# Performance work log

Measured on AMD Instinct MI355X. Metric: run time of the kernel, lower is better.

Reference implementation:

```python
import jax, jax.numpy as jnp
import numpy as np

B, S, DIM, NH, NKV, HD, HID, L, VOCAB = 1, 2048, 1024, 16, 8, 64, 2816, 2, 32000
EPS = 1e-5
SCALE = float(HD) ** 0.5
NEG = -255.0  # mask fill value used by executorch example inputs


def setup_inputs() -> dict:
    key = jax.random.key(0)
    ks = jax.random.split(key, 16)
    sd = 0.02
    def rnd(k, shape):
        return jax.random.normal(k, shape, dtype=jnp.float32) * sd
    # rope tables: precompute_freqs_cis(head_dim, max_seq_len)[: -1] -> [S, HD//2]
    inv = 1.0 / (10000.0 ** (np.arange(0, HD, 2, dtype=np.float32) / HD))
    ang = np.outer(np.arange(S, dtype=np.float32), inv)
    # causal mask [S, S]
    tril = np.tril(np.ones((S, S), dtype=bool))
    mask = np.where(tril, 0.0, NEG).astype(np.float32)
    return {
        "tokens": jax.random.randint(ks[0], (B, S), 0, VOCAB, dtype=jnp.int32),
        "atten_mask": jnp.asarray(mask),
        "freqs_cos": jnp.asarray(np.cos(ang)),
        "freqs_sin": jnp.asarray(np.sin(ang)),
        "tok_emb": rnd(ks[1], (VOCAB, DIM)),
        "wq": rnd(ks[2], (L, DIM, NH * HD)),
        "wk": rnd(ks[3], (L, DIM, NKV * HD)),
        "wv": rnd(ks[4], (L, DIM, NKV * HD)),
        "wo": rnd(ks[5], (L, NH * HD, DIM)),
        "attn_norm_w": jnp.ones((L, DIM), jnp.float32),
        "ffn_norm_w": jnp.ones((L, DIM), jnp.float32),
        "w1": rnd(ks[6], (L, DIM, HID)),
        "w2": rnd(ks[7], (L, HID, DIM)),
        "w3": rnd(ks[8], (L, DIM, HID)),
        "final_norm_w": jnp.ones((DIM,), jnp.float32),
        "out_w": rnd(ks[9], (DIM, VOCAB)),
    }


def _rmsnorm(x, w):
    return x * jax.lax.rsqrt(jnp.mean(x * x, axis=-1, keepdims=True) + EPS) * w


def _rope(x, c, s):
    # faithful to apply_rotary_emb_single: de-interleave, rotate, concat halves
    xr, xi = x[..., ::2], x[..., 1::2]          # [B,S,H,HD/2]
    c = c[None, :, None, :]
    s = s[None, :, None, :]
    return jnp.concatenate([xr * c - xi * s, xr * s + xi * c], axis=-1)


def reference(tokens, atten_mask, freqs_cos, freqs_sin, tok_emb, wq, wk, wv, wo,
              attn_norm_w, ffn_norm_w, w1, w2, w3, final_norm_w, out_w):
    rep = NH // NKV
    h = tok_emb[tokens]                           # [B,S,DIM]
    k_news, v_news = [], []
    for l in range(L):
        x = _rmsnorm(h, attn_norm_w[l])
        q = (x @ wq[l]).reshape(B, S, NH, HD)
        k = (x @ wk[l]).reshape(B, S, NKV, HD)
        v = (x @ wv[l]).reshape(B, S, NKV, HD)
        q = _rope(q, freqs_cos, freqs_sin)
        k = _rope(k, freqs_cos, freqs_sin)
        # GQA: each kv head serves NH//NKV query heads
        kr = jnp.repeat(k, rep, axis=2)           # [B,S,NH,HD]
        vr = jnp.repeat(v, rep, axis=2)
        attn = jnp.einsum('bshd,bthd->bhst', q, kr) / SCALE + atten_mask[None, None]
        p = jax.nn.softmax(attn, axis=-1)
        y = jnp.einsum('bhst,bthd->bshd', p, vr).reshape(B, S, NH * HD)
        h = h + y @ wo[l]
        x = _rmsnorm(h, ffn_norm_w[l])
        h = h + (jax.nn.silu(x @ w1[l]) * (x @ w3[l])) @ w2[l]
        # output_new_cache_only: last-position rotated K and raw V per kv head
        k_news.append(k[:, -1])                   # [B,NKV,HD]
        v_news.append(v[:, -1])
    logits = _rmsnorm(h, final_norm_w) @ out_w    # [B,S,VOCAB]
    return logits, jnp.stack(k_news), jnp.stack(v_news)
```

## Files before the change

### kernel.cpp

```cpp
#include <hip/hip_runtime.h>
#include <hip/hip_bf16.h>

typedef __bf16 bf16x8 __attribute__((ext_vector_type(8)));
typedef float f32x4 __attribute__((ext_vector_type(4)));
typedef unsigned short ushort4v __attribute__((ext_vector_type(4)));
typedef unsigned short ushort8v __attribute__((ext_vector_type(8)));

#define S_LEN 2048
#define DIM 1024
#define NH 16
#define NKV 8
#define HD 64
#define HID 2816
#define LOGITS ((size_t)S_LEN * 32000)

__device__ __forceinline__ unsigned short f2bf(float f) {
    union { float f; unsigned u; } v; v.f = f;
    unsigned r = v.u + 0x7fffu + ((v.u >> 16) & 1u);
    return (unsigned short)(r >> 16);
}
__device__ __forceinline__ float bf2f(unsigned short u) {
    union { unsigned u; float f; } v; v.u = (unsigned)u << 16; return v.f;
}

__device__ __forceinline__ void gload16(const unsigned short* g, unsigned short* l) {
    __builtin_amdgcn_global_load_lds(
        (const __attribute__((address_space(1))) unsigned int*)g,
        (__attribute__((address_space(3))) unsigned int*)l,
        16, 0, 0);
}

union Frag { f32x4 f; bf16x8 h; };

__device__ __forceinline__ f32x4 lds_read_b128(unsigned addr) {
    f32x4 d;
    asm volatile("ds_read_b128 %0, %1" : "=v"(d) : "v"(addr));
    return d;
}

#define BAR()  asm volatile("s_barrier" ::: "memory")
#define WAITV(n) asm volatile("s_waitcnt vmcnt(" #n ")" ::: "memory")
#define LGKM0() do { asm volatile("s_waitcnt lgkmcnt(0)" ::: "memory"); __builtin_amdgcn_sched_barrier(0); } while (0)

__global__ __launch_bounds__(256) void embed_kernel(const int* __restrict__ tokens,
                                                    const float* __restrict__ emb,
                                                    float* __restrict__ h) {
    int s = blockIdx.x;
    int t = tokens[s];
    float4 v = *(const float4*)&emb[(size_t)t * DIM + threadIdx.x * 4];
    *(float4*)&h[(size_t)s * DIM + threadIdx.x * 4] = v;
}

__global__ __launch_bounds__(256) void rmsnorm_kernel(const float* __restrict__ x,
                                                      const float* __restrict__ w,
                                                      unsigned short* __restrict__ out) {
    __shared__ float sred[4];
    int s = blockIdx.x;
    int tid = threadIdx.x;
    float4 v = *(const float4*)&x[(size_t)s * DIM + tid * 4];
    float ss = v.x * v.x + v.y * v.y + v.z * v.z + v.w * v.w;
#pragma unroll
    for (int off = 32; off; off >>= 1) ss += __shfl_down(ss, off);
    if ((tid & 63) == 0) sred[tid >> 6] = ss;
    __syncthreads();
    float tot = sred[0] + sred[1] + sred[2] + sred[3];
    float scale = rsqrtf(tot * (1.0f / DIM) + 1e-5f);
    float4 wv = *(const float4*)&w[tid * 4];
    ushort4v o;
    o[0] = f2bf(v.x * scale * wv.x); o[1] = f2bf(v.y * scale * wv.y);
    o[2] = f2bf(v.z * scale * wv.z); o[3] = f2bf(v.w * scale * wv.w);
    *(ushort4v*)&out[(size_t)s * DIM + tid * 4] = o;
}

__device__ __forceinline__ void tpose_body(const float* __restrict__ in,
                                           unsigned short* __restrict__ out,
                                           int K, int N, int n0, int k0,
                                           int rowMul, int rowOff) {
    __shared__ unsigned short t[64][68];
    int tid = threadIdx.x;
    int tn = tid & 15, tk = tid >> 4;
#pragma unroll
    for (int p = 0; p < 4; ++p) {
        int k = tk + p * 16;
        float4 v = *(const float4*)&in[(size_t)(k0 + k) * N + n0 + tn * 4];
        t[tn * 4 + 0][k] = f2bf(v.x);
        t[tn * 4 + 1][k] = f2bf(v.y);
        t[tn * 4 + 2][k] = f2bf(v.z);
        t[tn * 4 + 3][k] = f2bf(v.w);
    }
    __syncthreads();
    int wk = tid & 15, wn = tid >> 4;
#pragma unroll
    for (int p = 0; p < 4; ++p) {
        int n = wn + p * 16;
        ushort4v v;
        v[0] = t[n][wk * 4]; v[1] = t[n][wk * 4 + 1];
        v[2] = t[n][wk * 4 + 2]; v[3] = t[n][wk * 4 + 3];
        *(ushort4v*)&out[(size_t)(rowMul * (n0 + n) + rowOff) * K + k0 + wk * 4] = v;
    }
}

__global__ __launch_bounds__(256) void transpose_w(const float* __restrict__ in,
                                                   unsigned short* __restrict__ out,
                                                   int K, int N) {
    tpose_body(in, out, K, N, blockIdx.x * 64, blockIdx.y * 64, 1, 0);
}

__global__ __launch_bounds__(256) void transpose_layer(const float* __restrict__ wq,
                                                       const float* __restrict__ wk,
                                                       const float* __restrict__ wv,
                                                       const float* __restrict__ wo,
                                                       const float* __restrict__ w1,
                                                       const float* __restrict__ w3,
                                                       const float* __restrict__ w2,
                                                       unsigned short* __restrict__ wTqkv,
                                                       unsigned short* __restrict__ wTo,
                                                       unsigned short* __restrict__ wT13,
                                                       unsigned short* __restrict__ wT2) {
    int id = blockIdx.x;
    if (id < 256) {
        tpose_body(wq, wTqkv, 1024, 1024, (id & 15) * 64, (id >> 4) * 64, 1, 0);
    } else if (id < 384) {
        int i = id - 256;
        tpose_body(wk, wTqkv, 1024, 512, (i & 7) * 64, (i >> 3) * 64, 1, 1024);
    } else if (id < 512) {
        int i = id - 384;
        tpose_body(wv, wTqkv, 1024, 512, (i & 7) * 64, (i >> 3) * 64, 1, 1536);
    } else if (id < 768) {
        int i = id - 512;
        tpose_body(wo, wTo, 1024, 1024, (i & 15) * 64, (i >> 4) * 64, 1, 0);
    } else if (id < 1472) {
        int i = id - 768;
        tpose_body(w1, wT13, 1024, HID, (i % 44) * 64, (i / 44) * 64, 2, 0);
    } else if (id < 2176) {
        int i = id - 1472;
        tpose_body(w3, wT13, 1024, HID, (i % 44) * 64, (i / 44) * 64, 2, 1);
    } else {
        int i = id - 2176;
        tpose_body(w2, wT2, 2816, 1024, (i & 15) * 64, (i >> 4) * 64, 1, 0);
    }
}

__global__ __launch_bounds__(256) void gemm_qkv(const unsigned short* __restrict__ A,
                                                const unsigned short* __restrict__ Bt,
                                                const float* __restrict__ fc,
                                                const float* __restrict__ fs,
                                                unsigned short* __restrict__ qb,
                                                unsigned short* __restrict__ kb,
                                                unsigned short* __restrict__ vT,
                                                float* __restrict__ out, int layer) {
    __shared__ unsigned short As[2][128 * 64];
    __shared__ unsigned short Bs[2][128 * 64];
    const int K = DIM, lda = DIM;
    int tid = threadIdx.x;
    int lane = tid & 63;
    int wid = tid >> 6;
    int wrow = wid >> 1, wcol = wid & 1;
    int lr = lane & 15, lg = lane >> 4;
    const int m0 = blockIdx.x * 128, n0 = blockIdx.y * 128;

    const int col8 = (((lane & 7) ^ ((lane >> 3) & 7)) * 8);
    const unsigned short* aG = A + (size_t)(m0 + wid * 32 + (lane >> 3)) * lda + col8;
    const unsigned short* bG = Bt + (size_t)(n0 + wid * 32 + (lane >> 3)) * K + col8;
    const int NT = K >> 6;

#define STG128(buf, k0) do {                                                  \
        unsigned short* _aL = &As[buf][wid * 2048];                           \
        unsigned short* _bL = &Bs[buf][wid * 2048];                           \
        _Pragma("unroll")                                                     \
        for (int _i = 0; _i < 4; ++_i) {                                      \
            gload16(aG + (size_t)(_i * 8) * lda + (k0), _aL + _i * 512);      \
            gload16(bG + (size_t)(_i * 8) * K + (k0), _bL + _i * 512);        \
        }                                                                     \
    } while (0)

    f32x4 acc[4][4] = {};
    STG128(0, 0);
    WAITV(0);
    BAR();

    for (int t = 0; t < NT; ++t) {
        int buf = t & 1;
        if (t + 1 < NT) STG128(buf ^ 1, (t + 1) * 64);
#pragma unroll
        for (int kk = 0; kk < 2; ++kk) {
            const int slot = ((kk * 4 + lg) ^ (lr & 7)) * 8;
            bf16x8 aF[4], bF[4];
#pragma unroll
            for (int mi = 0; mi < 4; ++mi)
                aF[mi] = *(const bf16x8*)&As[buf][(wrow * 64 + mi * 16 + lr) * 64 + slot];
#pragma unroll
            for (int ni = 0; ni < 4; ++ni)
                bF[ni] = *(const bf16x8*)&Bs[buf][(wcol * 64 + ni * 16 + lr) * 64 + slot];
#pragma unroll
            for (int mi = 0; mi < 4; ++mi)
#pragma unroll
                for (int ni = 0; ni < 4; ++ni)
                    acc[mi][ni] = __builtin_amdgcn_mfma_f32_16x16x32_bf16(aF[mi], bF[ni], acc[mi][ni], 0, 0, 0);
        }
        if (t + 1 < NT) WAITV(0);
        BAR();
    }
#undef STG128

#pragma unroll
    for (int mi = 0; mi < 4; ++mi)
#pragma unroll
        for (int ni = 0; ni < 4; ++ni) {
            int col = n0 + wcol * 64 + ni * 16 + lr;
            int s0r = m0 + wrow * 64 + mi * 16 + lg * 4;
            if (col < 1536) {
                int p = (col & 63) >> 1;
                int odd = col & 1;
#pragma unroll
                for (int r = 0; r < 4; ++r) {
                    float v = acc[mi][ni][r];
                    float o = __shfl_xor(v, 1);
                    int s = s0r + r;
                    float c = fc[s * 32 + p], sn = fs[s * 32 + p];
                    float res = odd ? (o * sn + v * c) : (v * c - o * sn);
                    int dpos = (odd ? 32 : 0) + p;
                    if (col < 1024) {
                        qb[(size_t)s * 1024 + (col >> 6) * 64 + dpos] = f2bf(res);
                    } else {
                        int kcol = ((col >> 6) - 16) * 64 + dpos;
                        kb[(size_t)s * 512 + kcol] = f2bf(res);
                        if (s == S_LEN - 1)
                            out[LOGITS + (size_t)layer * 512 + kcol] = res;
                    }
                }
            } else {
                int d = col - 1536;
                ushort4v vv;
#pragma unroll
                for (int r = 0; r < 4; ++r) vv[r] = f2bf(acc[mi][ni][r]);
                *(ushort4v*)&vT[(size_t)d * 2048 + s0r] = vv;
                if (s0r + 3 == S_LEN - 1)
                    out[LOGITS + 2 * 512 + (size_t)layer * 512 + d] = acc[mi][ni][3];
            }
        }
}

template<int FUSE>
__global__ __launch_bounds__(256) void gemm_tn128(const unsigned short* __restrict__ A, int lda,
                                                  const unsigned short* __restrict__ Bt,
                                                  float* __restrict__ Cf,
                                                  unsigned short* __restrict__ Cb,
                                                  const float* __restrict__ addsrc,
                                                  int N, int K) {
    __shared__ unsigned short As[2][128 * 64];
    __shared__ unsigned short Bs[2][128 * 64];
    int tid = threadIdx.x;
    int lane = tid & 63;
    int wid = tid >> 6;
    int wrow = wid >> 1, wcol = wid & 1;
    int lr = lane & 15, lg = lane >> 4;
    const int m0 = blockIdx.x * 128, n0 = blockIdx.y * 128;

    const int col8 = (((lane & 7) ^ ((lane >> 3) & 7)) * 8);
    const unsigned short* aG = A + (size_t)(m0 + wid * 32 + (lane >> 3)) * lda + col8;
    const unsigned short* bG = Bt + (size_t)(n0 + wid * 32 + (lane >> 3)) * K + col8;
    const int NT = K >> 6;

#define STG128(buf, k0) do {                                                  \
        unsigned short* _aL = &As[buf][wid * 2048];                           \
        unsigned short* _bL = &Bs[buf][wid * 2048];                           \
        _Pragma("unroll")                                                     \
        for (int _i = 0; _i < 4; ++_i) {                                      \
            gload16(aG + (size_t)(_i * 8) * lda + (k0), _aL + _i * 512);      \
            gload16(bG + (size_t)(_i * 8) * K + (k0), _bL + _i * 512);        \
        }                                                                     \
    } while (0)

    f32x4 acc[4][4] = {};
    STG128(0, 0);
    WAITV(0);
    BAR();

    for (int t = 0; t < NT; ++t) {
        int buf = t & 1;
        if (t + 1 < NT) STG128(buf ^ 1, (t + 1) * 64);
#pragma unroll
        for (int kk = 0; kk < 2; ++kk) {
            const int slot = ((kk * 4 + lg) ^ (lr & 7)) * 8;
            bf16x8 aF[4], bF[4];
#pragma unroll
            for (int mi = 0; mi < 4; ++mi)
                aF[mi] = *(const bf16x8*)&As[buf][(wrow * 64 + mi * 16 + lr) * 64 + slot];
#pragma unroll
            for (int ni = 0; ni < 4; ++ni)
                bF[ni] = *(const bf16x8*)&Bs[buf][(wcol * 64 + ni * 16 + lr) * 64 + slot];
#pragma unroll
            for (int mi = 0; mi < 4; ++mi)
#pragma unroll
                for (int ni = 0; ni < 4; ++ni)
                    acc[mi][ni] = __builtin_amdgcn_mfma_f32_16x16x32_bf16(aF[mi], bF[ni], acc[mi][ni], 0, 0, 0);
        }
        if (t + 1 < NT) WAITV(0);
        BAR();
    }
#undef STG128

#pragma unroll
    for (int mi = 0; mi < 4; ++mi)
#pragma unroll
        for (int ni = 0; ni < 4; ++ni) {
            int row = m0 + wrow * 64 + mi * 16 + lg * 4;
            int col = n0 + wcol * 64 + ni * 16 + lr;
#pragma unroll
            for (int r = 0; r < 4; ++r) {
                float v = acc[mi][ni][r];
                if (FUSE) {
                    float o = __shfl_xor(v, 1);
                    if (!(lr & 1))
                        Cb[(size_t)(row + r) * HID + (col >> 1)] = f2bf(v / (1.f + __expf(-v)) * o);
                } else {
                    size_t idx = (size_t)(row + r) * N + col;
                    if (addsrc) v += addsrc[idx];
                    if (Cb) Cb[idx] = f2bf(v);
                    else    Cf[idx] = v;
                }
            }
        }
}

__global__ __launch_bounds__(256) void gemm_tn64(const unsigned short* __restrict__ A, int lda,
                                                 const unsigned short* __restrict__ Bt,
                                                 float* __restrict__ Cf,
                                                 const float* __restrict__ addsrc,
                                                 int N, int K) {
    __shared__ unsigned short As[2][64 * 64];
    __shared__ unsigned short Bs[2][128 * 64];
    int tid = threadIdx.x;
    int lane = tid & 63;
    int wid = tid >> 6;
    int lr = lane & 15, lg = lane >> 4;
    const int m0 = blockIdx.x * 64, n0 = blockIdx.y * 128;

    const int srow = tid >> 3;
    const int col8 = (((tid & 7) ^ ((tid >> 3) & 7)) * 8);
    const unsigned short* aG = A + (size_t)(m0 + srow) * lda + col8;
    const unsigned short* bG = Bt + (size_t)(n0 + srow) * K + col8;
    const int NT = K >> 6;

#define STG64(buf, k0) do {                                                   \
        gload16(aG + (k0), &As[buf][wid * 512]);                              \
        gload16(aG + (size_t)32 * lda + (k0), &As[buf][wid * 512 + 2048]);    \
        _Pragma("unroll")                                                     \
        for (int _i = 0; _i < 4; ++_i)                                        \
            gload16(bG + (size_t)(_i * 32) * K + (k0), &Bs[buf][wid * 512 + _i * 2048]); \
    } while (0)

    f32x4 acc[4][2] = {};
    STG64(0, 0);
    WAITV(0);
    BAR();

    for (int t = 0; t < NT; ++t) {
        int buf = t & 1;
        if (t + 1 < NT) STG64(buf ^ 1, (t + 1) * 64);
#pragma unroll
        for (int kk = 0; kk < 2; ++kk) {
            const int slot = ((kk * 4 + lg) ^ (lr & 7)) * 8;
            bf16x8 aF[4], bF[2];
#pragma unroll
            for (int mi = 0; mi < 4; ++mi)
                aF[mi] = *(const bf16x8*)&As[buf][(mi * 16 + lr) * 64 + slot];
#pragma unroll
            for (int ni = 0; ni < 2; ++ni)
                bF[ni] = *(const bf16x8*)&Bs[buf][(wid * 32 + ni * 16 + lr) * 64 + slot];
#pragma unroll
            for (int mi = 0; mi < 4; ++mi)
#pragma unroll
                for (int ni = 0; ni < 2; ++ni)
                    acc[mi][ni] = __builtin_amdgcn_mfma_f32_16x16x32_bf16(aF[mi], bF[ni], acc[mi][ni], 0, 0, 0);
        }
        if (t + 1 < NT) WAITV(0);
        BAR();
    }
#undef STG64

#pragma unroll
    for (int mi = 0; mi < 4; ++mi)
#pragma unroll
        for (int ni = 0; ni < 2; ++ni) {
            int row = m0 + mi * 16 + lg * 4;
            int col = n0 + wid * 32 + ni * 16 + lr;
#pragma unroll
            for (int r = 0; r < 4; ++r) {
                size_t idx = (size_t)(row + r) * N + col;
                float v = acc[mi][ni][r];
                if (addsrc) v += addsrc[idx];
                Cf[idx] = v;
            }
        }
}

__global__ __launch_bounds__(512) void gemm8k32(const unsigned short* __restrict__ A,
                                                const unsigned short* __restrict__ Bt,
                                                float* __restrict__ Cf,
                                                int N, int K) {
    __shared__ unsigned short ldsbuf[32768];
    const int NT = K >> 5;
    int tid = threadIdx.x;
    int lane = tid & 63;
    int wid = tid >> 6;
    int wm = wid >> 2, wn = wid & 3;
    int lr = lane & 15, lg = lane >> 4;
    int wl = blockIdx.x * gridDim.y + blockIdx.y;
    const int m0 = (wl & 7) * 256, n0 = (wl >> 3) * 256;

    unsigned lds0 = (unsigned)(size_t)(__attribute__((address_space(3))) unsigned short*)ldsbuf;
    const unsigned xoff = (unsigned)((lg ^ ((lr >> 1) & 3)) * 16);
    const int gsw = (lane & 3) ^ ((lane >> 3) & 3);
    const int srow = wid * 16 + (lane >> 2);

#define STGA(t) do { \
        unsigned short* _l = ldsbuf + (((t) & 1) * 2 + 0) * 8192 + wid * 512; \
        const unsigned short* _g = A + (size_t)(m0 + srow) * K + (size_t)(t) * 32 + gsw * 8; \
        gload16(_g, _l); \
        gload16(_g + (size_t)128 * K, _l + 4096); \
    } while (0)
#define STGB(t) do { \
        unsigned short* _l = ldsbuf + (((t) & 1) * 2 + 1) * 8192 + wid * 512; \
        const unsigned short* _g = Bt + (size_t)(n0 + srow) * K + (size_t)(t) * 32 + gsw * 8; \
        gload16(_g, _l); \
        gload16(_g + (size_t)128 * K, _l + 4096); \
    } while (0)

    f32x4 acc[8][4] = {};

    STGA(0); STGB(0); STGB(1);
    WAITV(2);
    BAR();

    for (int t = 0; t < NT; ++t) {
        int buf = t & 1;
        unsigned aBase = lds0 + (unsigned)(buf * 32768) + (unsigned)((wm * 128 + lr) * 64) + xoff;
        unsigned bBase = lds0 + (unsigned)(buf * 32768 + 16384) + (unsigned)((wn * 64 + lr) * 64) + xoff;
        Frag aF[4], bF[4];
#pragma unroll
        for (int ni = 0; ni < 4; ++ni)
            bF[ni].f = lds_read_b128(bBase + (unsigned)(ni * 1024));
#pragma unroll
        for (int mi = 0; mi < 4; ++mi)
            aF[mi].f = lds_read_b128(aBase + (unsigned)(mi * 1024));
        if (t + 1 < NT) STGA(t + 1);
        BAR();
        LGKM0();
        __builtin_amdgcn_s_setprio(1);
#pragma unroll
        for (int mi = 0; mi < 4; ++mi)
#pragma unroll
            for (int ni = 0; ni < 4; ++ni)
                acc[mi][ni] = __builtin_amdgcn_mfma_f32_16x16x32_bf16(aF[mi].h, bF[ni].h, acc[mi][ni], 0, 0, 0);
        __builtin_amdgcn_s_setprio(0);
        BAR();
#pragma unroll
        for (int mi = 0; mi < 4; ++mi)
            aF[mi].f = lds_read_b128(aBase + (unsigned)(4096 + mi * 1024));
        if (t + 2 < NT) STGB(t + 2);
        BAR();
        LGKM0();
        __builtin_amdgcn_s_setprio(1);
#pragma unroll
        for (int mi = 0; mi < 4; ++mi)
#pragma unroll
            for (int ni = 0; ni < 4; ++ni)
                acc[4 + mi][ni] = __builtin_amdgcn_mfma_f32_16x16x32_bf16(aF[mi].h, bF[ni].h, acc[4 + mi][ni], 0, 0, 0);
        __builtin_amdgcn_s_setprio(0);
        if (t + 2 < NT)      { WAITV(2); }
        else if (t + 1 < NT) { WAITV(0); }
        BAR();
    }
#undef STGA
#undef STGB

#pragma unroll
    for (int mi = 0; mi < 8; ++mi)
#pragma unroll
        for (int ni = 0; ni < 4; ++ni) {
            int row = m0 + wm * 128 + mi * 16 + lg * 4;
            int col = n0 + wn * 64 + ni * 16 + lr;
#pragma unroll
            for (int r = 0; r < 4; ++r)
                Cf[(size_t)(row + r) * N + col] = acc[mi][ni][r];
        }
}

__global__ __launch_bounds__(256) void attn_kernel(const unsigned short* __restrict__ qb,
                                                   const unsigned short* __restrict__ kb,
                                                   const unsigned short* __restrict__ vT,
                                                   unsigned short* __restrict__ yb) {
    __shared__ unsigned short Klds[2][4096];
    __shared__ unsigned short Vlds[2][4096];
    __shared__ unsigned short P[4][16 * 72];
    int kvh = blockIdx.x;
    int strip = 63 - blockIdx.y;
    int tid = threadIdx.x;
    int lane = tid & 63;
    int w = tid >> 6;
    int hq = w & 1, qsub = w >> 1;
    int h = kvh * 2 + hq;
    int lr = lane & 15, lg = lane >> 4;
    int qbase = strip * 32 + qsub * 16;
    int qrow = qbase + lr;

    const int sr = tid >> 3;
    const int scol8 = (((tid & 7) ^ (sr & 7)) * 8);
    const int NT = (strip >> 1) + 1;

#define STAGEKV(buf, kt) do { \
        gload16(&kb[(size_t)((kt) * 64 + sr) * 512 + kvh * 64 + scol8], &Klds[buf][w * 512]); \
        gload16(&kb[(size_t)((kt) * 64 + sr + 32) * 512 + kvh * 64 + scol8], &Klds[buf][2048 + w * 512]); \
        gload16(&vT[(size_t)(kvh * 64 + sr) * 2048 + (kt) * 64 + scol8], &Vlds[buf][w * 512]); \
        gload16(&vT[(size_t)(kvh * 64 + sr + 32) * 2048 + (kt) * 64 + scol8], &Vlds[buf][2048 + w * 512]); \
    } while (0)

    bf16x8 bq[2];
#pragma unroll
    for (int c = 0; c < 2; ++c)
        bq[c] = *(const bf16x8*)&qb[(size_t)qrow * (NH * HD) + h * HD + c * 32 + lg * 8];

    f32x4 O[4] = {};
    float mstate = -1e30f, lstate = 0.f;

    STAGEKV(0, 0);
    WAITV(0);
    BAR();

    for (int kt = 0; kt < NT; ++kt) {
        int buf = kt & 1;
        if (kt + 1 < NT) STAGEKV(buf ^ 1, kt + 1);
        f32x4 s[4];
#pragma unroll
        for (int kc = 0; kc < 4; ++kc) {
            int krl = kc * 16 + lr;
            const unsigned short* kp = &Klds[buf][krl * 64];
            bf16x8 ak0 = *(const bf16x8*)&kp[((lg ^ (lr & 7)) * 8)];
            bf16x8 ak1 = *(const bf16x8*)&kp[(((4 + lg) ^ (lr & 7)) * 8)];
            f32x4 z = {};
            z = __builtin_amdgcn_mfma_f32_16x16x32_bf16(ak0, bq[0], z, 0, 0, 0);
            z = __builtin_amdgcn_mfma_f32_16x16x32_bf16(ak1, bq[1], z, 0, 0, 0);
            s[kc] = z;
        }
        float tm = -1e30f;
#pragma unroll
        for (int kc = 0; kc < 4; ++kc)
#pragma unroll
            for (int r = 0; r < 4; ++r) {
                int key = kt * 64 + kc * 16 + lg * 4 + r;
                float val = s[kc][r] * 0.125f;
                if (key > qrow) val = -1e30f;
                s[kc][r] = val;
                tm = fmaxf(tm, val);
            }
        tm = fmaxf(tm, __shfl_xor(tm, 16));
        tm = fmaxf(tm, __shfl_xor(tm, 32));
        float mn = fmaxf(mstate, tm);
        float sc = __expf(mstate - mn);
        float rs = 0.f;
        ushort4v pk[4];
#pragma unroll
        for (int kc = 0; kc < 4; ++kc)
#pragma unroll
            for (int r = 0; r < 4; ++r) {
                float pf = __expf(s[kc][r] - mn);
                rs += pf;
                pk[kc][r] = f2bf(pf);
            }
        rs += __shfl_xor(rs, 16);
        rs += __shfl_xor(rs, 32);
        lstate = lstate * sc + rs;
        mstate = mn;
        float osc[4];
#pragma unroll
        for (int r = 0; r < 4; ++r)
            osc[r] = __shfl(sc, lg * 4 + r);
#pragma unroll
        for (int n = 0; n < 4; ++n)
#pragma unroll
            for (int r = 0; r < 4; ++r)
                O[n][r] *= osc[r];
#pragma unroll
        for (int kc = 0; kc < 4; ++kc)
            *(ushort4v*)&P[w][lr * 72 + kc * 16 + lg * 4] = pk[kc];
        bf16x8 pa[2];
#pragma unroll
        for (int g = 0; g < 2; ++g)
            pa[g] = *(const bf16x8*)&P[w][lr * 72 + g * 32 + lg * 8];
#pragma unroll
        for (int n = 0; n < 4; ++n) {
            const unsigned short* vp = &Vlds[buf][(n * 16 + lr) * 64];
#pragma unroll
            for (int g = 0; g < 2; ++g) {
                bf16x8 bv = *(const bf16x8*)&vp[(((g * 4 + lg) ^ (lr & 7)) * 8)];
                O[n] = __builtin_amdgcn_mfma_f32_16x16x32_bf16(pa[g], bv, O[n], 0, 0, 0);
            }
        }
        if (kt + 1 < NT) WAITV(0);
        LGKM0();
        BAR();
    }
#undef STAGEKV

    float linv[4];
#pragma unroll
    for (int r = 0; r < 4; ++r)
        linv[r] = 1.f / __shfl(lstate, lg * 4 + r);
#pragma unroll
    for (int n = 0; n < 4; ++n)
#pragma unroll
        for (int r = 0; r < 4; ++r) {
            int row = qbase + lg * 4 + r;
            yb[(size_t)row * (NH * HD) + h * HD + n * 16 + lr] = f2bf(O[n][r] * linv[r]);
        }
}

extern "C" void kernel_launch(void* const* d_in, const int* in_sizes, int n_in,
                              void* d_out, int out_size, void* d_ws, size_t ws_size,
                              hipStream_t stream) {
    const int* tokens = (const int*)d_in[0];
    const float* freqs_cos = (const float*)d_in[2];
    const float* freqs_sin = (const float*)d_in[3];
    const float* tok_emb = (const float*)d_in[4];
    const float* wq = (const float*)d_in[5];
    const float* wk = (const float*)d_in[6];
    const float* wv = (const float*)d_in[7];
    const float* wo = (const float*)d_in[8];
    const float* attn_norm_w = (const float*)d_in[9];
    const float* ffn_norm_w = (const float*)d_in[10];
    const float* w1 = (const float*)d_in[11];
    const float* w2 = (const float*)d_in[12];
    const float* w3 = (const float*)d_in[13];
    const float* final_norm_w = (const float*)d_in[14];
    const float* out_w = (const float*)d_in[15];
    float* out = (float*)d_out;

    const size_t SD = (size_t)S_LEN * DIM;
    const size_t SKV = (size_t)S_LEN * NKV * HD;

    char* p = (char*)d_ws;
    auto take = [&](size_t bytes) { char* r = p; p += (bytes + 255) & ~(size_t)255; return r; };
    float* h            = (float*)take(SD * 4);
    unsigned short* xnb = (unsigned short*)take(SD * 2);
    char* uni = p;
    unsigned short* qb    = (unsigned short*)uni;
    unsigned short* kb    = qb + SD;
    unsigned short* vT    = kb + SKV;
    unsigned short* ybv   = vT + SKV;
    unsigned short* gu    = ybv + SD;
    unsigned short* wTqkv = gu + (size_t)S_LEN * HID;
    unsigned short* wTo   = wTqkv + (size_t)2048 * DIM;
    unsigned short* wT13  = wTo + (size_t)DIM * DIM;
    unsigned short* wT2   = wT13 + (size_t)2 * HID * DIM;
    unsigned short* owT   = (unsigned short*)uni;

    embed_kernel<<<S_LEN, 256, 0, stream>>>(tokens, tok_emb, h);
    for (int l = 0; l < 2; ++l) {
        rmsnorm_kernel<<<S_LEN, 256, 0, stream>>>(h, attn_norm_w + l * DIM, xnb);
        transpose_layer<<<2880, 256, 0, stream>>>(
            wq + (size_t)l * DIM * 1024, wk + (size_t)l * DIM * 512, wv + (size_t)l * DIM * 512,
            wo + (size_t)l * 1024 * DIM,
            w1 + (size_t)l * DIM * HID, w3 + (size_t)l * DIM * HID, w2 + (size_t)l * HID * 1024,
            wTqkv, wTo, wT13, wT2);
        gemm_qkv<<<dim3(16, 16), 256, 0, stream>>>(xnb, wTqkv, freqs_cos, freqs_sin,
                                                   qb, kb, vT, out, l);
        attn_kernel<<<dim3(NKV, 64), 256, 0, stream>>>(qb, kb, vT, ybv);
        gemm_tn64<<<dim3(32, 8), 256, 0, stream>>>(ybv, 1024, wTo, h, h, DIM, 1024);
        rmsnorm_kernel<<<S_LEN, 256, 0, stream>>>(h, ffn_norm_w + l * DIM, xnb);
        gemm_tn128<1><<<dim3(16, 44), 256, 0, stream>>>(xnb, DIM, wT13, nullptr, gu, nullptr, 5632, DIM);
        gemm_tn64<<<dim3(32, 8), 256, 0, stream>>>(gu, HID, wT2, h, h, DIM, HID);
    }
    rmsnorm_kernel<<<S_LEN, 256, 0, stream>>>(h, final_norm_w, xnb);
    transpose_w<<<dim3(500, 16), 256, 0, stream>>>(out_w, owT, DIM, 32000);
    gemm8k32<<<dim3(8, 125), 512, 0, stream>>>(xnb, owT, out, 32000, DIM);
}
```

Measured before the change: 631.5 us.

## Fuse weight transposes into co-scheduled rmsnorm and attention kernel launches

```diff
diff --git a/kernel.cpp b/kernel.cpp
--- a/kernel.cpp
+++ b/kernel.cpp
@@ -51,11 +51,10 @@
     *(float4*)&h[(size_t)s * DIM + threadIdx.x * 4] = v;
 }
 
-__global__ __launch_bounds__(256) void rmsnorm_kernel(const float* __restrict__ x,
-                                                      const float* __restrict__ w,
-                                                      unsigned short* __restrict__ out) {
+__device__ __forceinline__ void rmsnorm_body(const float* __restrict__ x,
+                                             const float* __restrict__ w,
+                                             unsigned short* __restrict__ out, int s) {
     __shared__ float sred[4];
-    int s = blockIdx.x;
     int tid = threadIdx.x;
     float4 v = *(const float4*)&x[(size_t)s * DIM + tid * 4];
     float ss = v.x * v.x + v.y * v.y + v.z * v.z + v.w * v.w;
@@ -72,6 +71,12 @@
     *(ushort4v*)&out[(size_t)s * DIM + tid * 4] = o;
 }
 
+__global__ __launch_bounds__(256) void rmsnorm_kernel(const float* __restrict__ x,
+                                                      const float* __restrict__ w,
+                                                      unsigned short* __restrict__ out) {
+    rmsnorm_body(x, w, out, blockIdx.x);
+}
+
 __device__ __forceinline__ void tpose_body(const float* __restrict__ in,
                                            unsigned short* __restrict__ out,
                                            int K, int N, int n0, int k0,
@@ -100,24 +105,12 @@
     }
 }
 
-__global__ __launch_bounds__(256) void transpose_w(const float* __restrict__ in,
-                                                   unsigned short* __restrict__ out,
-                                                   int K, int N) {
-    tpose_body(in, out, K, N, blockIdx.x * 64, blockIdx.y * 64, 1, 0);
-}
-
-__global__ __launch_bounds__(256) void transpose_layer(const float* __restrict__ wq,
-                                                       const float* __restrict__ wk,
-                                                       const float* __restrict__ wv,
-                                                       const float* __restrict__ wo,
-                                                       const float* __restrict__ w1,
-                                                       const float* __restrict__ w3,
-                                                       const float* __restrict__ w2,
-                                                       unsigned short* __restrict__ wTqkv,
-                                                       unsigned short* __restrict__ wTo,
-                                                       unsigned short* __restrict__ wT13,
-                                                       unsigned short* __restrict__ wT2) {
-    int id = blockIdx.x;
+__device__ __forceinline__ void tposeL_body(int id,
+                                            const float* wq, const float* wk, const float* wv,
+                                            const float* wo, const float* w1, const float* w3,
+                                            const float* w2,
+                                            unsigned short* wTqkv, unsigned short* wTo,
+                                            unsigned short* wT13, unsigned short* wT2) {
     if (id < 256) {
         tpose_body(wq, wTqkv, 1024, 1024, (id & 15) * 64, (id >> 4) * 64, 1, 0);
     } else if (id < 384) {
@@ -141,6 +134,174 @@
     }
 }
 
+__global__ __launch_bounds__(256) void rms_tposeL(const float* __restrict__ x,
+                                                  const float* __restrict__ nw,
+                                                  unsigned short* __restrict__ xnb,
+                                                  const float* wq, const float* wk, const float* wv,
+                                                  const float* wo, const float* w1, const float* w3,
+                                                  const float* w2,
+                                                  unsigned short* wTqkv, unsigned short* wTo,
+                                                  unsigned short* wT13, unsigned short* wT2) {
+    int id = blockIdx.x;
+    if (id < 2048) rmsnorm_body(x, nw, xnb, id);
+    else tposeL_body(id - 2048, wq, wk, wv, wo, w1, w3, w2, wTqkv, wTo, wT13, wT2);
+}
+
+__global__ __launch_bounds__(256) void rms_tposeO(const float* __restrict__ x,
+                                                  const float* __restrict__ nw,
+                                                  unsigned short* __restrict__ xnb,
+                                                  const float* __restrict__ out_w,
+                                                  unsigned short* __restrict__ owT) {
+    int id = blockIdx.x;
+    if (id < 2048) { rmsnorm_body(x, nw, xnb, id); return; }
+    int i = id - 2048;
+    tpose_body(out_w, owT, 1024, 32000, (i % 500) * 64, (i / 500) * 64, 1, 0);
+}
+
+__device__ __forceinline__ void attn_body(int id,
+                                          const unsigned short* __restrict__ qb,
+                                          const unsigned short* __restrict__ kb,
+                                          const unsigned short* __restrict__ vT,
+                                          unsigned short* __restrict__ yb) {
+    __shared__ unsigned short Klds[2][4096];
+    __shared__ unsigned short Vlds[2][4096];
+    __shared__ unsigned short P[4][16 * 72];
+    int kvh = id & 7;
+    int strip = 63 - (id >> 3);
+    int tid = threadIdx.x;
+    int lane = tid & 63;
+    int w = tid >> 6;
+    int hq = w & 1, qsub = w >> 1;
+    int h = kvh * 2 + hq;
+    int lr = lane & 15, lg = lane >> 4;
+    int qbase = strip * 32 + qsub * 16;
+    int qrow = qbase + lr;
+
+    const int sr = tid >> 3;
+    const int scol8 = (((tid & 7) ^ (sr & 7)) * 8);
+    const int NT = (strip >> 1) + 1;
+
+#define STAGEKV(buf, kt) do { \
+        gload16(&kb[(size_t)((kt) * 64 + sr) * 512 + kvh * 64 + scol8], &Klds[buf][w * 512]); \
+        gload16(&kb[(size_t)((kt) * 64 + sr + 32) * 512 + kvh * 64 + scol8], &Klds[buf][2048 + w * 512]); \
+        gload16(&vT[(size_t)(kvh * 64 + sr) * 2048 + (kt) * 64 + scol8], &Vlds[buf][w * 512]); \
+        gload16(&vT[(size_t)(kvh * 64 + sr + 32) * 2048 + (kt) * 64 + scol8], &Vlds[buf][2048 + w * 512]); \
+    } while (0)
+
+    bf16x8 bq[2];
+#pragma unroll
+    for (int c = 0; c < 2; ++c)
+        bq[c] = *(const bf16x8*)&qb[(size_t)qrow * (NH * HD) + h * HD + c * 32 + lg * 8];
+
+    f32x4 O[4] = {};
+    float mstate = -1e30f, lstate = 0.f;
+
+    STAGEKV(0, 0);
+    WAITV(0);
+    BAR();
+
+    for (int kt = 0; kt < NT; ++kt) {
+        int buf = kt & 1;
+        if (kt + 1 < NT) STAGEKV(buf ^ 1, kt + 1);
+        f32x4 s[4];
+#pragma unroll
+        for (int kc = 0; kc < 4; ++kc) {
+            int krl = kc * 16 + lr;
+            const unsigned short* kp = &Klds[buf][krl * 64];
+            bf16x8 ak0 = *(const bf16x8*)&kp[((lg ^ (lr & 7)) * 8)];
+            bf16x8 ak1 = *(const bf16x8*)&kp[(((4 + lg) ^ (lr & 7)) * 8)];
+            f32x4 z = {};
+            z = __builtin_amdgcn_mfma_f32_16x16x32_bf16(ak0, bq[0], z, 0, 0, 0);
+            z = __builtin_amdgcn_mfma_f32_16x16x32_bf16(ak1, bq[1], z, 0, 0, 0);
+            s[kc] = z;
+        }
+        float tm = -1e30f;
+#pragma unroll
+        for (int kc = 0; kc < 4; ++kc)
+#pragma unroll
+            for (int r = 0; r < 4; ++r) {
+                int key = kt * 64 + kc * 16 + lg * 4 + r;
+                float val = s[kc][r] * 0.125f;
+                if (key > qrow) val = -1e30f;
+                s[kc][r] = val;
+                tm = fmaxf(tm, val);
+            }
+        tm = fmaxf(tm, __shfl_xor(tm, 16));
+        tm = fmaxf(tm, __shfl_xor(tm, 32));
+        float mn = fmaxf(mstate, tm);
+        float sc = __expf(mstate - mn);
+        float rs = 0.f;
+        ushort4v pk[4];
+#pragma unroll
+        for (int kc = 0; kc < 4; ++kc)
+#pragma unroll
+            for (int r = 0; r < 4; ++r) {
+                float pf = __expf(s[kc][r] - mn);
+                rs += pf;
+                pk[kc][r] = f2bf(pf);
+            }
+        rs += __shfl_xor(rs, 16);
+        rs += __shfl_xor(rs, 32);
+        lstate = lstate * sc + rs;
+        mstate = mn;
+        float osc[4];
+#pragma unroll
+        for (int r = 0; r < 4; ++r)
+            osc[r] = __shfl(sc, lg * 4 + r);
+#pragma unroll
+        for (int n = 0; n < 4; ++n)
+#pragma unroll
+            for (int r = 0; r < 4; ++r)
+                O[n][r] *= osc[r];
+#pragma unroll
+        for (int kc = 0; kc < 4; ++kc)
+            *(ushort4v*)&P[w][lr * 72 + kc * 16 + lg * 4] = pk[kc];
+        bf16x8 pa[2];
+#pragma unroll
+        for (int g = 0; g < 2; ++g)
+            pa[g] = *(const bf16x8*)&P[w][lr * 72 + g * 32 + lg * 8];
+#pragma unroll
+        for (int n = 0; n < 4; ++n) {
+            const unsigned short* vp = &Vlds[buf][(n * 16 + lr) * 64];
+#pragma unroll
+            for (int g = 0; g < 2; ++g) {
+                bf16x8 bv = *(const bf16x8*)&vp[(((g * 4 + lg) ^ (lr & 7)) * 8)];
+                O[n] = __builtin_amdgcn_mfma_f32_16x16x32_bf16(pa[g], bv, O[n], 0, 0, 0);
+            }
+        }
+        if (kt + 1 < NT) WAITV(0);
+        LGKM0();
+        BAR();
+    }
+#undef STAGEKV
+
+    float linv[4];
+#pragma unroll
+    for (int r = 0; r < 4; ++r)
+        linv[r] = 1.f / __shfl(lstate, lg * 4 + r);
+#pragma unroll
+    for (int n = 0; n < 4; ++n)
+#pragma unroll
+        for (int r = 0; r < 4; ++r) {
+            int row = qbase + lg * 4 + r;
+            yb[(size_t)row * (NH * HD) + h * HD + n * 16 + lr] = f2bf(O[n][r] * linv[r]);
+        }
+}
+
+__global__ __launch_bounds__(256) void attn_tposeL(const unsigned short* __restrict__ qb,
+                                                   const unsigned short* __restrict__ kb,
+                                                   const unsigned short* __restrict__ vT,
+                                                   unsigned short* __restrict__ yb,
+                                                   const float* wq, const float* wk, const float* wv,
+                                                   const float* wo, const float* w1, const float* w3,
+                                                   const float* w2,
+                                                   unsigned short* wTqkv, unsigned short* wTo,
+                                                   unsigned short* wT13, unsigned short* wT2) {
+    int id = blockIdx.x;
+    if (id < 512) attn_body(id, qb, kb, vT, yb);
+    else tposeL_body(id - 512, wq, wk, wv, wo, w1, w3, w2, wTqkv, wTo, wT13, wT2);
+}
+
 __global__ __launch_bounds__(256) void gemm_qkv(const unsigned short* __restrict__ A,
                                                 const unsigned short* __restrict__ Bt,
                                                 const float* __restrict__ fc,
@@ -488,135 +649,6 @@
         }
 }
 
-__global__ __launch_bounds__(256) void attn_kernel(const unsigned short* __restrict__ qb,
-                                                   const unsigned short* __restrict__ kb,
-                                                   const unsigned short* __restrict__ vT,
-                                                   unsigned short* __restrict__ yb) {
-    __shared__ unsigned short Klds[2][4096];
-    __shared__ unsigned short Vlds[2][4096];
-    __shared__ unsigned short P[4][16 * 72];
-    int kvh = blockIdx.x;
-    int strip = 63 - blockIdx.y;
-    int tid = threadIdx.x;
-    int lane = tid & 63;
-    int w = tid >> 6;
-    int hq = w & 1, qsub = w >> 1;
-    int h = kvh * 2 + hq;
-    int lr = lane & 15, lg = lane >> 4;
-    int qbase = strip * 32 + qsub * 16;
-    int qrow = qbase + lr;
-
-    const int sr = tid >> 3;
-    const int scol8 = (((tid & 7) ^ (sr & 7)) * 8);
-    const int NT = (strip >> 1) + 1;
-
-#define STAGEKV(buf, kt) do { \
-        gload16(&kb[(size_t)((kt) * 64 + sr) * 512 + kvh * 64 + scol8], &Klds[buf][w * 512]); \
-        gload16(&kb[(size_t)((kt) * 64 + sr + 32) * 512 + kvh * 64 + scol8], &Klds[buf][2048 + w * 512]); \
-        gload16(&vT[(size_t)(kvh * 64 + sr) * 2048 + (kt) * 64 + scol8], &Vlds[buf][w * 512]); \
-        gload16(&vT[(size_t)(kvh * 64 + sr + 32) * 2048 + (kt) * 64 + scol8], &Vlds[buf][2048 + w * 512]); \
-    } while (0)
-
-    bf16x8 bq[2];
-#pragma unroll
-    for (int c = 0; c < 2; ++c)
-        bq[c] = *(const bf16x8*)&qb[(size_t)qrow * (NH * HD) + h * HD + c * 32 + lg * 8];
-
-    f32x4 O[4] = {};
-    float mstate = -1e30f, lstate = 0.f;
-
-    STAGEKV(0, 0);
-    WAITV(0);
-    BAR();
-
-    for (int kt = 0; kt < NT; ++kt) {
-        int buf = kt & 1;
-        if (kt + 1 < NT) STAGEKV(buf ^ 1, kt + 1);
-        f32x4 s[4];
-#pragma unroll
-        for (int kc = 0; kc < 4; ++kc) {
-            int krl = kc * 16 + lr;
-            const unsigned short* kp = &Klds[buf][krl * 64];
-            bf16x8 ak0 = *(const bf16x8*)&kp[((lg ^ (lr & 7)) * 8)];
-            bf16x8 ak1 = *(const bf16x8*)&kp[(((4 + lg) ^ (lr & 7)) * 8)];
-            f32x4 z = {};
-            z = __builtin_amdgcn_mfma_f32_16x16x32_bf16(ak0, bq[0], z, 0, 0, 0);
-            z = __builtin_amdgcn_mfma_f32_16x16x32_bf16(ak1, bq[1], z, 0, 0, 0);
-            s[kc] = z;
-        }
-        float tm = -1e30f;
-#pragma unroll
-        for (int kc = 0; kc < 4; ++kc)
-#pragma unroll
-            for (int r = 0; r < 4; ++r) {
-                int key = kt * 64 + kc * 16 + lg * 4 + r;
-                float val = s[kc][r] * 0.125f;
-                if (key > qrow) val = -1e30f;
-                s[kc][r] = val;
-                tm = fmaxf(tm, val);
-            }
-        tm = fmaxf(tm, __shfl_xor(tm, 16));
-        tm = fmaxf(tm, __shfl_xor(tm, 32));
-        float mn = fmaxf(mstate, tm);
-        float sc = __expf(mstate - mn);
-        float rs = 0.f;
-        ushort4v pk[4];
-#pragma unroll
-        for (int kc = 0; kc < 4; ++kc)
-#pragma unroll
-            for (int r = 0; r < 4; ++r) {
-                float pf = __expf(s[kc][r] - mn);
-                rs += pf;
-                pk[kc][r] = f2bf(pf);
-            }
-        rs += __shfl_xor(rs, 16);
-        rs += __shfl_xor(rs, 32);
-        lstate = lstate * sc + rs;
-        mstate = mn;
-        float osc[4];
-#pragma unroll
-        for (int r = 0; r < 4; ++r)
-            osc[r] = __shfl(sc, lg * 4 + r);
-#pragma unroll
-        for (int n = 0; n < 4; ++n)
-#pragma unroll
-            for (int r = 0; r < 4; ++r)
-                O[n][r] *= osc[r];
-#pragma unroll
-        for (int kc = 0; kc < 4; ++kc)
-            *(ushort4v*)&P[w][lr * 72 + kc * 16 + lg * 4] = pk[kc];
-        bf16x8 pa[2];
-#pragma unroll
-        for (int g = 0; g < 2; ++g)
-            pa[g] = *(const bf16x8*)&P[w][lr * 72 + g * 32 + lg * 8];
-#pragma unroll
-        for (int n = 0; n < 4; ++n) {
-            const unsigned short* vp = &Vlds[buf][(n * 16 + lr) * 64];
-#pragma unroll
-            for (int g = 0; g < 2; ++g) {
-                bf16x8 bv = *(const bf16x8*)&vp[(((g * 4 + lg) ^ (lr & 7)) * 8)];
-                O[n] = __builtin_amdgcn_mfma_f32_16x16x32_bf16(pa[g], bv, O[n], 0, 0, 0);
-            }
-        }
-        if (kt + 1 < NT) WAITV(0);
-        LGKM0();
-        BAR();
-    }
-#undef STAGEKV
-
-    float linv[4];
-#pragma unroll
-    for (int r = 0; r < 4; ++r)
-        linv[r] = 1.f / __shfl(lstate, lg * 4 + r);
-#pragma unroll
-    for (int n = 0; n < 4; ++n)
-#pragma unroll
-        for (int r = 0; r < 4; ++r) {
-            int row = qbase + lg * 4 + r;
-            yb[(size_t)row * (NH * HD) + h * HD + n * 16 + lr] = f2bf(O[n][r] * linv[r]);
-        }
-}
-
 extern "C" void kernel_launch(void* const* d_in, const int* in_sizes, int n_in,
                               void* d_out, int out_size, void* d_ws, size_t ws_size,
                               hipStream_t stream) {
@@ -650,29 +682,37 @@
     unsigned short* vT    = kb + SKV;
     unsigned short* ybv   = vT + SKV;
     unsigned short* gu    = ybv + SD;
-    unsigned short* wTqkv = gu + (size_t)S_LEN * HID;
-    unsigned short* wTo   = wTqkv + (size_t)2048 * DIM;
-    unsigned short* wT13  = wTo + (size_t)DIM * DIM;
-    unsigned short* wT2   = wT13 + (size_t)2 * HID * DIM;
-    unsigned short* owT   = (unsigned short*)uni;
+    unsigned short* wTqkv0 = gu + (size_t)S_LEN * HID;
+    unsigned short* wTo0   = wTqkv0 + (size_t)2048 * DIM;
+    unsigned short* wT13_0 = wTo0 + (size_t)DIM * DIM;
+    unsigned short* wT2_0  = wT13_0 + (size_t)2 * HID * DIM;
+    unsigned short* wTqkv1 = wT2_0 + (size_t)DIM * HID;
+    unsigned short* wTo1   = wTqkv1 + (size_t)2048 * DIM;
+    unsigned short* wT13_1 = wTo1 + (size_t)DIM * DIM;
+    unsigned short* wT2_1  = wT13_1 + (size_t)2 * HID * DIM;
+    unsigned short* owT    = (unsigned short*)uni;
 
     embed_kernel<<<S_LEN, 256, 0, stream>>>(tokens, tok_emb, h);
-    for (int l = 0; l < 2; ++l) {
-        rmsnorm_kernel<<<S_LEN, 256, 0, stream>>>(h, attn_norm_w + l * DIM, xnb);
-        transpose_layer<<<2880, 256, 0, stream>>>(
-            wq + (size_t)l * DIM * 1024, wk + (size_t)l * DIM * 512, wv + (size_t)l * DIM * 512,
-            wo + (size_t)l * 1024 * DIM,
-            w1 + (size_t)l * DIM * HID, w3 + (size_t)l * DIM * HID, w2 + (size_t)l * HID * 1024,
-            wTqkv, wTo, wT13, wT2);
-        gemm_qkv<<<dim3(16, 16), 256, 0, stream>>>(xnb, wTqkv, freqs_cos, freqs_sin,
-                                                   qb, kb, vT, out, l);
-        attn_kernel<<<dim3(NKV, 64), 256, 0, stream>>>(qb, kb, vT, ybv);
-        gemm_tn64<<<dim3(32, 8), 256, 0, stream>>>(ybv, 1024, wTo, h, h, DIM, 1024);
-        rmsnorm_kernel<<<S_LEN, 256, 0, stream>>>(h, ffn_norm_w + l * DIM, xnb);
-        gemm_tn128<1><<<dim3(16, 44), 256, 0, stream>>>(xnb, DIM, wT13, nullptr, gu, nullptr, 5632, DIM);
-        gemm_tn64<<<dim3(32, 8), 256, 0, stream>>>(gu, HID, wT2, h, h, DIM, HID);
-    }
-    rmsnorm_kernel<<<S_LEN, 256, 0, stream>>>(h, final_norm_w, xnb);
-    transpose_w<<<dim3(500, 16), 256, 0, stream>>>(out_w, owT, DIM, 32000);
+    rms_tposeL<<<2048 + 2880, 256, 0, stream>>>(h, attn_norm_w, xnb,
+        wq, wk, wv, wo, w1, w3, w2, wTqkv0, wTo0, wT13_0, wT2_0);
+    gemm_qkv<<<dim3(16, 16), 256, 0, stream>>>(xnb, wTqkv0, freqs_cos, freqs_sin, qb, kb, vT, out, 0);
+    attn_tposeL<<<512 + 2880, 256, 0, stream>>>(qb, kb, vT, ybv,
+        wq + (size_t)DIM * 1024, wk + (size_t)DIM * 512, wv + (size_t)DIM * 512,
+        wo + (size_t)1024 * DIM, w1 + (size_t)DIM * HID, w3 + (size_t)DIM * HID,
+        w2 + (size_t)HID * 1024, wTqkv1, wTo1, wT13_1, wT2_1);
+    gemm_tn64<<<dim3(32, 8), 256, 0, stream>>>(ybv, 1024, wTo0, h, h, DIM, 1024);
+    rmsnorm_kernel<<<S_LEN, 256, 0, stream>>>(h, ffn_norm_w, xnb);
+    gemm_tn128<1><<<dim3(16, 44), 256, 0, stream>>>(xnb, DIM, wT13_0, nullptr, gu, nullptr, 5632, DIM);
+    gemm_tn64<<<dim3(32, 8), 256, 0, stream>>>(gu, HID, wT2_0, h, h, DIM, HID);
+    rmsnorm_kernel<<<S_LEN, 256, 0, stream>>>(h, attn_norm_w + DIM, xnb);
+    gemm_qkv<<<dim3(16, 16), 256, 0, stream>>>(xnb, wTqkv1, freqs_cos, freqs_sin, qb, kb, vT, out, 1);
+    attn_tposeL<<<512, 256, 0, stream>>>(qb, kb, vT, ybv,
+        nullptr, nullptr, nullptr, nullptr, nullptr, nullptr, nullptr,
+        nullptr, nullptr, nullptr, nullptr);
+    gemm_tn64<<<dim3(32, 8), 256, 0, stream>>>(ybv, 1024, wTo1, h, h, DIM, 1024);
+    rmsnorm_kernel<<<S_LEN, 256, 0, stream>>>(h, ffn_norm_w + DIM, xnb);
+    gemm_tn128<1><<<dim3(16, 44), 256, 0, stream>>>(xnb, DIM, wT13_1, nullptr, gu, nullptr, 5632, DIM);
+    gemm_tn64<<<dim3(32, 8), 256, 0, stream>>>(gu, HID, wT2_1, h, h, DIM, HID);
+    rms_tposeO<<<2048 + 8000, 256, 0, stream>>>(h, final_norm_w, xnb, out_w, owT);
     gemm8k32<<<dim3(8, 125), 512, 0, stream>>>(xnb, owT, out, 32000, DIM);
 }
```

New measurement: 608.4 us (median of 2 runs). 3.7% less time.
